# Kernel tuning notes

Measured on AMD Instinct MI355X. Metric: run time of the kernel, lower is better.

The kernel has to match this reference:

```python
import jax, jax.numpy as jnp
import numpy as np

B, P_LEN, Q_LEN, D, H = 16, 128, 256, 128, 128


def setup_inputs() -> dict:
    key = jax.random.key(0)
    ks = jax.random.split(key, 16)
    s = 0.05
    inp = {
        "p": jax.random.normal(ks[0], (B, P_LEN, D), dtype=jnp.float32),
        "q": jax.random.normal(ks[1], (B, Q_LEN, D), dtype=jnp.float32),
        # attention linears: W_s, W_t (D->H), W_r (H->H), W_e (H->1)
        "Ws_w": jax.random.normal(ks[2], (H, D), dtype=jnp.float32) * s,
        "Ws_b": jnp.zeros((H,), dtype=jnp.float32),
        "Wt_w": jax.random.normal(ks[3], (H, D), dtype=jnp.float32) * s,
        "Wt_b": jnp.zeros((H,), dtype=jnp.float32),
        "Wr_w": jax.random.normal(ks[4], (H, H), dtype=jnp.float32) * s,
        "Wr_b": jnp.zeros((H,), dtype=jnp.float32),
        "We_w": jax.random.normal(ks[5], (H,), dtype=jnp.float32) * s,
        "We_b": jax.random.normal(ks[6], (), dtype=jnp.float32) * s,
        # input gate linear: (D+H)->(D+H)
        "Wg_w": jax.random.normal(ks[7], (D + H, D + H), dtype=jnp.float32) * s,
        "Wg_b": jnp.zeros((D + H,), dtype=jnp.float32),
        # LSTMCell: gates ordered i,f,g,o as in torch
        "Wih": jax.random.normal(ks[8], (4 * H, D + H), dtype=jnp.float32) * s,
        "Whh": jax.random.normal(ks[9], (4 * H, H), dtype=jnp.float32) * s,
        "bih": jnp.zeros((4 * H,), dtype=jnp.float32),
        "bhh": jnp.zeros((4 * H,), dtype=jnp.float32),
        # entity_embedding=None -> these int ids are unused pass-throughs
        "p_seq": jax.random.randint(ks[10], (B, P_LEN), 0, 10000, dtype=jnp.int64) if jax.config.jax_enable_x64 else jax.random.randint(ks[10], (B, P_LEN), 0, 10000, dtype=jnp.int32),
        "q_seq": jax.random.randint(ks[11], (B, Q_LEN), 0, 10000, dtype=jnp.int32),
    }
    return inp


def _mlstm(p, q, Ws_w, Ws_b, Wt_w, Wt_b, Wr_w, Wr_b, We_w, We_b,
           Wg_w, Wg_b, Wih, Whh, bih, bhh):
    # precompute W_s(q): [B, Q, H] (loop-invariant)
    W_hs = jnp.einsum('bqd,hd->bqh', q, Ws_w) + Ws_b
    h0 = jnp.zeros((p.shape[0], H), dtype=p.dtype)
    c0 = jnp.zeros_like(h0)

    def step(carry, p_pos):  # p_pos: [B, D]
        h, c = carry
        # TriMatchAttention (entity_embedding=None)
        w_ht = p_pos @ Wt_w.T + Wt_b            # [B, H]
        w_hm = h @ Wr_w.T + Wr_b                # [B, H]
        s = jnp.tanh(W_hs + (w_ht + w_hm)[:, None, :])   # [B, Q, H]
        score = jnp.einsum('bqh,h->bq', s, We_w) + We_b  # [B, Q]
        a = jax.nn.softmax(score, axis=1)                # [B, Q]
        alpha = jnp.einsum('bq,bqh->bh', a, W_hs)        # [B, H]
        x = jnp.concatenate([alpha, p_pos], axis=1)      # [B, H+D]
        # gate (IsGate=True)
        g_t = jax.nn.sigmoid(x @ Wg_w.T + Wg_b)
        x = g_t * x
        # LSTMCell
        gates = x @ Wih.T + bih + h @ Whh.T + bhh        # [B, 4H]
        i, f, g, o = jnp.split(gates, 4, axis=1)
        c_new = jax.nn.sigmoid(f) * c + jax.nn.sigmoid(i) * jnp.tanh(g)
        h_new = jax.nn.sigmoid(o) * jnp.tanh(c_new)
        return (h_new, c_new), h_new

    _, hs = jax.lax.scan(step, (h0, c0), jnp.swapaxes(p, 0, 1))  # hs: [P, B, H]
    return jnp.swapaxes(hs, 0, 1)  # [B, P, H] == stacked h_states[1:]


def reference(p, q, Ws_w, Ws_b, Wt_w, Wt_b, Wr_w, Wr_b, We_w, We_b,
              Wg_w, Wg_b, Wih, Whh, bih, bhh, p_seq, q_seq):
    # p_seq/q_seq unused: entity_embedding=None in TriMatchAttention
    return _mlstm(p, q, Ws_w, Ws_b, Wt_w, Wt_b, Wr_w, Wr_b, We_w, We_b,
                  Wg_w, Wg_b, Wih, Whh, bih, bhh)
```

## Files before the change

### kernel.cpp

```cpp
#include <hip/hip_runtime.h>
#include <hip/hip_fp16.h>
#include <cstdint>


__device__ __forceinline__ float bf2f(uint16_t u) {
  uint32_t x = ((uint32_t)u) << 16; float f; __builtin_memcpy(&f, &x, 4); return f;
}
__device__ __forceinline__ float load_in(const void* p, size_t i, int f32) {
  return f32 ? ((const float*)p)[i] : bf2f(((const uint16_t*)p)[i]);
}
__device__ __forceinline__ float frcp(float x) { return __builtin_amdgcn_rcpf(x); }
__device__ __forceinline__ float tanh_fast(float x) {
  float E = __expf(2.0f * x);
  return 1.0f - 2.0f * frcp(E + 1.0f);
}
__device__ __forceinline__ float sigm(float x) { return frcp(1.0f + __expf(-x)); }
__device__ __forceinline__ float2 h2f(uint32_t u) {
  __half2 h; __builtin_memcpy(&h, &u, 4); return __half22float2(h);
}
__device__ __forceinline__ uint32_t f2h(float a, float b) {
  __half2 h = __floats2half2_rn(a, b);
  uint32_t u; __builtin_memcpy(&u, &h, 4); return u;
}

__global__ void detect_kernel(const uint16_t* __restrict__ q16,
                              uint32_t* __restrict__ flag) {
  __shared__ int cnt;
  if (threadIdx.x == 0) cnt = 0;
  __syncthreads();
  int bad = 0;
  for (int i = threadIdx.x; i < 4096; i += 256) {
    int e = (q16[i] >> 7) & 0xFF;
    if (e > 0x8A) bad++;
  }
  atomicAdd(&cnt, bad);
  __syncthreads();
  if (threadIdx.x == 0) *flag = (cnt > 16) ? 1u : 0u;
}

__global__ void pack2(const void* __restrict__ p,
                      const void* __restrict__ Wr,  const void* __restrict__ Wrb_,
                      const void* __restrict__ Wew_, const void* __restrict__ Web_,
                      const void* __restrict__ Wg,
                      const void* __restrict__ Wih, const void* __restrict__ Whh,
                      const void* __restrict__ bih, const void* __restrict__ bhh,
                      float* __restrict__ pf,
                      uint32_t* __restrict__ WrP, float* __restrict__ wrb,
                      float* __restrict__ wew, float* __restrict__ web,
                      uint32_t* __restrict__ WgP, uint32_t* __restrict__ WTP,
                      float* __restrict__ bbv,
                      const uint32_t* __restrict__ flag) {
  const int f32 = (int)*flag;
  long idx = (long)blockIdx.x * blockDim.x + threadIdx.x;
  if (idx < 262144) { pf[idx] = load_in(p, idx, f32); return; }
  idx -= 262144;
  if (idx < 8192) {
    int c = (int)(idx >> 2), w = (int)(idx & 3);
    int i = c >> 10, t = c & 1023;
    int jA = t >> 3, kgA = t & 7;
    int k = kgA * 16 + i * 8 + w * 2;
    WrP[idx] = f2h(load_in(Wr, (size_t)jA * 128 + k, f32),
                   load_in(Wr, (size_t)jA * 128 + k + 1, f32));
    return; }
  idx -= 8192;
  if (idx < 128) { wrb[idx] = load_in(Wrb_, idx, f32); return; }
  idx -= 128;
  if (idx < 128) { wew[idx] = load_in(Wew_, idx, f32); return; }
  idx -= 128;
  if (idx < 1) { web[0] = load_in(Web_, 0, f32); return; }
  idx -= 1;
  if (idx < 16384) {
    int c = (int)(idx >> 2), w = (int)(idx & 3);
    int i = c >> 10, t = c & 1023;
    int iE = t >> 2, kgE = t & 3;
    int k = kgE * 32 + i * 8 + w * 2;
    WgP[idx] = f2h(load_in(Wg, (size_t)iE * 256 + k, f32),
                   load_in(Wg, (size_t)iE * 256 + k + 1, f32));
    return; }
  idx -= 16384;
  if (idx < 98304) {
    int c = (int)(idx >> 2), w = (int)(idx & 3);
    int i = c >> 10, t = c & 1023;
    int iF = t >> 1, kgF = t & 1;
    int k = kgF * 192 + i * 8 + w * 2;
    float v0 = (k < 256) ? load_in(Wih, (size_t)iF * 256 + k, f32)
                         : load_in(Whh, (size_t)iF * 128 + (k - 256), f32);
    float v1 = (k + 1 < 256) ? load_in(Wih, (size_t)iF * 256 + k + 1, f32)
                             : load_in(Whh, (size_t)iF * 128 + (k + 1 - 256), f32);
    WTP[idx] = f2h(v0, v1);
    return; }
  idx -= 98304;
  if (idx < 512) { bbv[idx] = load_in(bih, idx, f32) + load_in(bhh, idx, f32); }
}

__global__ __launch_bounds__(256) void gemm3(
    const void* __restrict__ q, const void* __restrict__ p,
    const void* __restrict__ Wsw, const void* __restrict__ Wsb,
    const void* __restrict__ Wtw, const void* __restrict__ Wtb,
    const void* __restrict__ Wgw, const void* __restrict__ Wgb,
    float* __restrict__ whs, float* __restrict__ wht, float* __restrict__ Gp,
    const uint32_t* __restrict__ flag) {
  __shared__ float A_l[16][128];
  __shared__ float W_l[64][129];
  const int f32 = (int)*flag;
  const int t = threadIdx.x;
  const void* A; const void* W; const void* bias; float* out;
  int lda = 128, ldw, w_off, C, r0;
  int blk = blockIdx.x;
  if (blk < 256)      { A = q; W = Wsw; bias = Wsb; out = whs; ldw = 128; w_off = 0;   C = 128; r0 = blk * 16; }
  else if (blk < 384) { A = p; W = Wtw; bias = Wtb; out = wht; ldw = 128; w_off = 0;   C = 128; r0 = (blk - 256) * 16; }
  else                { A = p; W = Wgw; bias = Wgb; out = Gp;  ldw = 256; w_off = 128; C = 256; r0 = (blk - 384) * 16; }
  for (int idx = t; idx < 16 * 128; idx += 256) {
    int rr = idx >> 7, kk = idx & 127;
    A_l[rr][kk] = load_in(A, (size_t)(r0 + rr) * lda + kk, f32);
  }
  const int c_l = t & 63, rg = t >> 6;
  for (int c0 = 0; c0 < C; c0 += 64) {
    __syncthreads();
    for (int idx = t; idx < 64 * 128; idx += 256) {
      int cc = idx >> 7, kk = idx & 127;
      W_l[cc][kk] = load_in(W, (size_t)w_off + (size_t)(c0 + cc) * ldw + kk, f32);
    }
    __syncthreads();
    float acc[4] = {0.f, 0.f, 0.f, 0.f};
    for (int k = 0; k < 128; k++) {
      float w = W_l[c_l][k];
#pragma unroll
      for (int x = 0; x < 4; x++) acc[x] = fmaf(A_l[rg * 4 + x][k], w, acc[x]);
    }
    float bv = load_in(bias, c0 + c_l, f32);
#pragma unroll
    for (int x = 0; x < 4; x++)
      out[(size_t)(r0 + rg * 4 + x) * C + c0 + c_l] = acc[x] + bv;
  }
}

__global__ void tapack(const float* __restrict__ whs, uint32_t* __restrict__ TAp) {
  int o = blockIdx.x * 256 + threadIdx.x;
  int b = o >> 14, r = o & 16383;
  int c = r >> 2, w = r & 3;
  int i = c >> 10, t = c & 1023;
  int qB = t >> 2, hgB = t & 3;
  int h = hgB * 32 + i * 8 + w * 2;
  const float* base = whs + ((size_t)b * 256 + qB) * 128 + h;
  TAp[o] = f2h(tanhf(base[0]), tanhf(base[1]));
}

#define TUIDX(j) ((((j) >> 5) * 36) + ((j) & 31))
#define SCIDX(q) ((((q) >> 5) * 36) + ((q) & 31))
#define AIDX(h)  ((((h) >> 5) * 36) + ((h) & 31))
#define HIDX(k)  ((((k) >> 4) * 20) + ((k) & 15))

__global__ __launch_bounds__(1024) void mlstm_seq9(
    const float* __restrict__ pf,
    const float* __restrict__ whs,
    const float* __restrict__ wht_g,
    const float* __restrict__ Gp_g,
    const uint32_t* __restrict__ WrP,
    const float* __restrict__ wrb,
    const float* __restrict__ wew,
    const float* __restrict__ web,
    const uint32_t* __restrict__ WgP,
    const uint32_t* __restrict__ WTP,
    const uint32_t* __restrict__ TAp,
    const float* __restrict__ bbv,
    float* __restrict__ out) {
  const int b = blockIdx.x, t = threadIdx.x;

  __shared__ __align__(16) float whs_l[256 * 132];
  __shared__ __align__(16) float tu_s[144];
  __shared__ __align__(16) float wew_s[144];
  __shared__ __align__(16) float sc_s[288];
  __shared__ __align__(16) float e_s[256];
  __shared__ __align__(16) float alpha_s[144];
  __shared__ __align__(16) float xh_s[384];
  __shared__ __align__(16) float h_s[160];
  __shared__ __align__(16) float gates_s[512];
  __shared__ float inv_s;

  const float* whs_b = whs + (size_t)b * 32768;

  const int jA = t >> 3, kgA = t & 7;
  const int qB = t >> 2, hgB = t & 3;
  const int hD = t >> 3, qgD = t & 7;
  const int iE = t >> 2, kgE = t & 3;
  const int iF = t >> 1, kgF = t & 1;

  for (int i4 = t; i4 < 8192; i4 += 1024)
    *(float4*)(whs_l + (i4 >> 5) * 132 + ((i4 & 31) << 2)) =
        *(const float4*)(whs_b + ((size_t)i4 << 2));
  if (t < 128) wew_s[TUIDX(t)] = wew[t];
  if (t < 160) h_s[t] = 0.f;
  if (t < 128) xh_s[256 + t] = 0.f;

  const float wrb_r = wrb[jA];
  const float web_r = web[0];
  const float bbF_r = bbv[iF];
  float c_r = 0.f;

  const uint4* wrp4 = (const uint4*)WrP;
  const uint4* wgp4 = (const uint4*)WgP;
  const uint4* wtp4 = (const uint4*)WTP;
  const uint4* tap4 = (const uint4*)TAp + (size_t)b * 4096;

  float wht_c = (kgA == 0) ? wht_g[((size_t)b * 128 + 0) * 128 + jA] : 0.f;
  float gp_c  = (kgE == 0) ? Gp_g[((size_t)b * 128 + 0) * 256 + iE] : 0.f;
  float pf_c  = (kgE == 0 && iE >= 128) ? pf[((size_t)b * 128 + 0) * 128 + (iE - 128)] : 0.f;

  __syncthreads();

  for (int st = 0; st < 128; st++) {
    const int st1 = (st < 127) ? st + 1 : 127;
    float wht_n = (kgA == 0) ? wht_g[((size_t)b * 128 + st1) * 128 + jA] : 0.f;
    float gp_n  = (kgE == 0) ? Gp_g[((size_t)b * 128 + st1) * 256 + iE] : 0.f;
    float pf_n  = (kgE == 0 && iE >= 128) ? pf[((size_t)b * 128 + st1) * 128 + (iE - 128)] : 0.f;

    {
      float acc = 0.f;
#pragma unroll
      for (int i = 0; i < 2; i++) {
        uint4 wv = wrp4[i * 1024 + t];
        const float* hp = h_s + kgA * 20 + i * 8;
        float4 hA = *(const float4*)(hp);
        float4 hB = *(const float4*)(hp + 4);
        float2 w0 = h2f(wv.x), w1 = h2f(wv.y), w2 = h2f(wv.z), w3 = h2f(wv.w);
        acc = fmaf(hA.x, w0.x, acc); acc = fmaf(hA.y, w0.y, acc);
        acc = fmaf(hA.z, w1.x, acc); acc = fmaf(hA.w, w1.y, acc);
        acc = fmaf(hB.x, w2.x, acc); acc = fmaf(hB.y, w2.y, acc);
        acc = fmaf(hB.z, w3.x, acc); acc = fmaf(hB.w, w3.y, acc);
      }
      acc += __shfl_xor(acc, 1);
      acc += __shfl_xor(acc, 2);
      acc += __shfl_xor(acc, 4);
      if (kgA == 0) tu_s[TUIDX(jA)] = tanh_fast(acc + wrb_r + wht_c);
    }
    __syncthreads();

    {
      float acc = 0.f;
#pragma unroll
      for (int i = 0; i < 4; i++) {
        uint4 av = tap4[i * 1024 + t];
        const float* up = tu_s + hgB * 36 + i * 8;
        const float* wp = wew_s + hgB * 36 + i * 8;
        float4 uA = *(const float4*)(up);
        float4 uB = *(const float4*)(up + 4);
        float4 wA = *(const float4*)(wp);
        float4 wB = *(const float4*)(wp + 4);
        float2 a0 = h2f(av.x), a1 = h2f(av.y), a2 = h2f(av.z), a3 = h2f(av.w);
        acc = fmaf((a0.x + uA.x) * frcp(fmaxf(fmaf(a0.x, uA.x, 1.f), 1e-6f)), wA.x, acc);
        acc = fmaf((a0.y + uA.y) * frcp(fmaxf(fmaf(a0.y, uA.y, 1.f), 1e-6f)), wA.y, acc);
        acc = fmaf((a1.x + uA.z) * frcp(fmaxf(fmaf(a1.x, uA.z, 1.f), 1e-6f)), wA.z, acc);
        acc = fmaf((a1.y + uA.w) * frcp(fmaxf(fmaf(a1.y, uA.w, 1.f), 1e-6f)), wA.w, acc);
        acc = fmaf((a2.x + uB.x) * frcp(fmaxf(fmaf(a2.x, uB.x, 1.f), 1e-6f)), wB.x, acc);
        acc = fmaf((a2.y + uB.y) * frcp(fmaxf(fmaf(a2.y, uB.y, 1.f), 1e-6f)), wB.y, acc);
        acc = fmaf((a3.x + uB.z) * frcp(fmaxf(fmaf(a3.x, uB.z, 1.f), 1e-6f)), wB.z, acc);
        acc = fmaf((a3.y + uB.w) * frcp(fmaxf(fmaf(a3.y, uB.w, 1.f), 1e-6f)), wB.w, acc);
      }
      acc += __shfl_xor(acc, 1);
      acc += __shfl_xor(acc, 2);
      if (hgB == 0) sc_s[SCIDX(qB)] = acc + web_r;
    }
    __syncthreads();

    if (t < 64) {
      float s0 = sc_s[SCIDX(t)],       s1 = sc_s[SCIDX(t + 64)];
      float s2 = sc_s[SCIDX(t + 128)], s3 = sc_s[SCIDX(t + 192)];
      float mx = fmaxf(fmaxf(s0, s1), fmaxf(s2, s3));
#pragma unroll
      for (int d = 1; d < 64; d <<= 1) mx = fmaxf(mx, __shfl_xor(mx, d));
      float e0 = __expf(s0 - mx), e1 = __expf(s1 - mx),
            e2 = __expf(s2 - mx), e3 = __expf(s3 - mx);
      float sum = e0 + e1 + e2 + e3;
#pragma unroll
      for (int d = 1; d < 64; d <<= 1) sum += __shfl_xor(sum, d);
      e_s[t] = e0; e_s[t + 64] = e1; e_s[t + 128] = e2; e_s[t + 192] = e3;
      if (t == 0) inv_s = frcp(sum);
    }
    __syncthreads();

    {
      const float* whs_p = whs_l + qgD * 132 + hD;
      float acc = 0.f;
#pragma unroll 8
      for (int r = 0; r < 32; r++)
        acc = fmaf(e_s[qgD + 8 * r], whs_p[r * 1056], acc);
      acc += __shfl_xor(acc, 1);
      acc += __shfl_xor(acc, 2);
      acc += __shfl_xor(acc, 4);
      if (qgD == 0) alpha_s[AIDX(hD)] = acc * inv_s;
    }
    __syncthreads();

    {
      float acc = 0.f;
#pragma unroll
      for (int i = 0; i < 4; i++) {
        uint4 wv = wgp4[i * 1024 + t];
        const float* ap = alpha_s + kgE * 36 + i * 8;
        float4 aA = *(const float4*)(ap);
        float4 aB = *(const float4*)(ap + 4);
        float2 w0 = h2f(wv.x), w1 = h2f(wv.y), w2 = h2f(wv.z), w3 = h2f(wv.w);
        acc = fmaf(aA.x, w0.x, acc); acc = fmaf(aA.y, w0.y, acc);
        acc = fmaf(aA.z, w1.x, acc); acc = fmaf(aA.w, w1.y, acc);
        acc = fmaf(aB.x, w2.x, acc); acc = fmaf(aB.y, w2.y, acc);
        acc = fmaf(aB.z, w3.x, acc); acc = fmaf(aB.w, w3.y, acc);
      }
      acc += __shfl_xor(acc, 1);
      acc += __shfl_xor(acc, 2);
      if (kgE == 0) {
        float sg = sigm(gp_c + acc);
        float xv = (iE < 128) ? alpha_s[AIDX(iE)] : pf_c;
        xh_s[iE] = sg * xv;
      }
    }
    __syncthreads();

    {
      const float* xb = xh_s + kgF * 192;
      float acc = 0.f;
#pragma unroll 8
      for (int i = 0; i < 24; i++) {
        uint4 wv = wtp4[i * 1024 + t];
        float4 xA = *(const float4*)(xb + i * 8);
        float4 xB = *(const float4*)(xb + i * 8 + 4);
        float2 w0 = h2f(wv.x), w1 = h2f(wv.y), w2 = h2f(wv.z), w3 = h2f(wv.w);
        acc = fmaf(xA.x, w0.x, acc); acc = fmaf(xA.y, w0.y, acc);
        acc = fmaf(xA.z, w1.x, acc); acc = fmaf(xA.w, w1.y, acc);
        acc = fmaf(xB.x, w2.x, acc); acc = fmaf(xB.y, w2.y, acc);
        acc = fmaf(xB.z, w3.x, acc); acc = fmaf(xB.w, w3.y, acc);
      }
      acc += __shfl_xor(acc, 1);
      if (kgF == 0) gates_s[iF] = acc + bbF_r;
    }
    __syncthreads();

    if (t < 128) {
      float iv = sigm(gates_s[t]);
      float fv = sigm(gates_s[128 + t]);
      float gv = tanh_fast(gates_s[256 + t]);
      float ov = sigm(gates_s[384 + t]);
      float cn = fmaf(fv, c_r, iv * gv);
      float hn = ov * tanh_fast(cn);
      c_r = cn;
      h_s[HIDX(t)] = hn;
      xh_s[256 + t] = hn;
      out[((size_t)b * 128 + st) * 128 + t] = hn;
    }
    __syncthreads();

    wht_c = wht_n; gp_c = gp_n; pf_c = pf_n;
  }
}

extern "C" void kernel_launch(void* const* d_in, const int* in_sizes, int n_in,
                              void* d_out, int out_size, void* d_ws, size_t ws_size,
                              hipStream_t stream) {
  static const int SZ_DICT[18] = {262144, 524288, 16384, 128, 16384, 128,
                                  16384, 128, 128, 1, 65536, 256,
                                  131072, 65536, 512, 512, 2048, 4096};
  static const int ALPHA2DICT[18] = {9, 8, 11, 10, 13, 12, 7, 6, 3, 2, 5, 4,
                                     15, 14, 0, 16, 1, 17};
  const void* in[18];
  for (int i = 0; i < 18; i++) in[i] = (i < n_in) ? d_in[i] : nullptr;

  bool dict_ok = true;
  int lim = (n_in < 16) ? n_in : 16;
  for (int i = 0; i < lim; i++) if (in_sizes[i] != SZ_DICT[i]) dict_ok = false;
  if (!dict_ok) {
    bool alpha_ok = true;
    for (int s = 0; s < n_in && s < 18; s++)
      if (in_sizes[s] != SZ_DICT[ALPHA2DICT[s]]) alpha_ok = false;
    if (alpha_ok)
      for (int s = 0; s < n_in && s < 18; s++) in[ALPHA2DICT[s]] = d_in[s];
  }

  const void* p   = in[0];  const void* q   = in[1];
  const void* Wsw = in[2];  const void* Wsb = in[3];
  const void* Wtw = in[4];  const void* Wtb = in[5];
  const void* Wrw = in[6];  const void* Wrb = in[7];
  const void* Wew = in[8];  const void* Web = in[9];
  const void* Wgw = in[10]; const void* Wgb = in[11];
  const void* Wih = in[12]; const void* Whh = in[13];
  const void* bih = in[14]; const void* bhh = in[15];

  float* ws = (float*)d_ws;
  float* whs  = ws;
  float* pff  = whs + 524288;
  float* wht  = pff + 262144;
  float* Gp   = wht + 262144;
  uint32_t* WrP = (uint32_t*)(Gp + 524288);
  uint32_t* WgP = WrP + 8192;
  uint32_t* WTP = WgP + 16384;
  uint32_t* TAp = WTP + 98304;
  float* bbv  = (float*)(TAp + 262144);
  float* wrb  = bbv + 512;
  float* wew  = wrb + 128;
  float* web  = wew + 128;
  uint32_t* flag = (uint32_t*)(web + 4);

  hipLaunchKernelGGL(detect_kernel, dim3(1), dim3(256), 0, stream,
                     (const uint16_t*)q, flag);
  hipLaunchKernelGGL(pack2, dim3(1508), dim3(256), 0, stream,
                     p, Wrw, Wrb, Wew, Web, Wgw, Wih, Whh, bih, bhh,
                     pff, WrP, wrb, wew, web, WgP, WTP, bbv, flag);
  hipLaunchKernelGGL(gemm3, dim3(512), dim3(256), 0, stream,
                     q, p, Wsw, Wsb, Wtw, Wtb, Wgw, Wgb, whs, wht, Gp, flag);
  hipLaunchKernelGGL(tapack, dim3(1024), dim3(256), 0, stream, whs, TAp);
  hipLaunchKernelGGL(mlstm_seq9, dim3(16), dim3(1024), 0, stream,
                     pff, whs, wht, Gp, WrP, wrb, wew, web, WgP, WTP, TAp, bbv,
                     (float*)d_out);
}
```

Baseline: 1.420 ms.

## Pack W_hs to fp16 in global, cache LSTM weights in LDS, use fdot2

The sequential kernel no longer stages fp32 W_hs in LDS. It reads a pre-packed fp16 copy (DWp, produced by the extended pack kernel) for the alpha reduction. The freed LDS holds 9 of the 24 LSTM weight chunks, and the remaining chunks are software-prefetched from global. The gate input vector is stored as half2 so the LSTM matvec can use packed fp16 dot2 instructions. This cuts per-step global and LDS traffic and ALU work on the serial critical path, at the cost of fp16 rounding of activations and an extra packing pass.

```diff
diff --git a/kernel.cpp b/kernel.cpp
--- a/kernel.cpp
+++ b/kernel.cpp
@@ -21,6 +21,22 @@
 __device__ __forceinline__ uint32_t f2h(float a, float b) {
   __half2 h = __floats2half2_rn(a, b);
   uint32_t u; __builtin_memcpy(&u, &h, 4); return u;
+}
+
+typedef _Float16 h2v __attribute__((ext_vector_type(2)));
+__device__ __forceinline__ float dot2(uint32_t w, uint32_t x, float acc) {
+#if defined(__has_builtin)
+#if __has_builtin(__builtin_amdgcn_fdot2)
+  h2v a, b; __builtin_memcpy(&a, &w, 4); __builtin_memcpy(&b, &x, 4);
+  return __builtin_amdgcn_fdot2(a, b, acc, false);
+#else
+  float2 af = h2f(w), bf = h2f(x);
+  return fmaf(af.x, bf.x, fmaf(af.y, bf.y, acc));
+#endif
+#else
+  float2 af = h2f(w), bf = h2f(x);
+  return fmaf(af.x, bf.x, fmaf(af.y, bf.y, acc));
+#endif
 }
 
 __global__ void detect_kernel(const uint16_t* __restrict__ q16,
@@ -135,15 +151,27 @@
   }
 }
 
-__global__ void tapack(const float* __restrict__ whs, uint32_t* __restrict__ TAp) {
+__global__ void actpack(const float* __restrict__ whs,
+                        uint32_t* __restrict__ TAp, uint32_t* __restrict__ DWp) {
   int o = blockIdx.x * 256 + threadIdx.x;
-  int b = o >> 14, r = o & 16383;
-  int c = r >> 2, w = r & 3;
-  int i = c >> 10, t = c & 1023;
-  int qB = t >> 2, hgB = t & 3;
-  int h = hgB * 32 + i * 8 + w * 2;
-  const float* base = whs + ((size_t)b * 256 + qB) * 128 + h;
-  TAp[o] = f2h(tanhf(base[0]), tanhf(base[1]));
+  if (o < 262144) {
+    int b = o >> 14, r = o & 16383;
+    int c = r >> 2, w = r & 3;
+    int i = c >> 10, t = c & 1023;
+    int qB = t >> 2, hgB = t & 3;
+    int h = hgB * 32 + i * 8 + w * 2;
+    const float* base = whs + ((size_t)b * 256 + qB) * 128 + h;
+    TAp[o] = f2h(tanhf(base[0]), tanhf(base[1]));
+  } else {
+    o -= 262144;
+    int b = o >> 14, r2 = o & 16383;
+    int i = r2 >> 12, r = r2 & 4095;
+    int t = r >> 2, w = r & 3;
+    int qgD = t & 7, hD = t >> 3;
+    int q0 = qgD + 64 * i + 16 * w;
+    const float* base = whs + (size_t)b * 32768;
+    DWp[o] = f2h(base[(size_t)q0 * 128 + hD], base[(size_t)(q0 + 8) * 128 + hD]);
+  }
 }
 
 #define TUIDX(j) ((((j) >> 5) * 36) + ((j) & 31))
@@ -151,9 +179,8 @@
 #define AIDX(h)  ((((h) >> 5) * 36) + ((h) & 31))
 #define HIDX(k)  ((((k) >> 4) * 20) + ((k) & 15))
 
-__global__ __launch_bounds__(1024) void mlstm_seq9(
+__global__ __launch_bounds__(1024) void mlstm_seq10(
     const float* __restrict__ pf,
-    const float* __restrict__ whs,
     const float* __restrict__ wht_g,
     const float* __restrict__ Gp_g,
     const uint32_t* __restrict__ WrP,
@@ -163,22 +190,21 @@
     const uint32_t* __restrict__ WgP,
     const uint32_t* __restrict__ WTP,
     const uint32_t* __restrict__ TAp,
+    const uint32_t* __restrict__ DWp,
     const float* __restrict__ bbv,
     float* __restrict__ out) {
   const int b = blockIdx.x, t = threadIdx.x;
 
-  __shared__ __align__(16) float whs_l[256 * 132];
+  __shared__ __align__(16) uint4 lds_wt4[9 * 1024];
+  __shared__ __align__(16) uint32_t xh_h2[192];
   __shared__ __align__(16) float tu_s[144];
   __shared__ __align__(16) float wew_s[144];
   __shared__ __align__(16) float sc_s[288];
   __shared__ __align__(16) float e_s[256];
   __shared__ __align__(16) float alpha_s[144];
-  __shared__ __align__(16) float xh_s[384];
   __shared__ __align__(16) float h_s[160];
   __shared__ __align__(16) float gates_s[512];
   __shared__ float inv_s;
-
-  const float* whs_b = whs + (size_t)b * 32768;
 
   const int jA = t >> 3, kgA = t & 7;
   const int qB = t >> 2, hgB = t & 3;
@@ -186,22 +212,21 @@
   const int iE = t >> 2, kgE = t & 3;
   const int iF = t >> 1, kgF = t & 1;
 
-  for (int i4 = t; i4 < 8192; i4 += 1024)
-    *(float4*)(whs_l + (i4 >> 5) * 132 + ((i4 & 31) << 2)) =
-        *(const float4*)(whs_b + ((size_t)i4 << 2));
+  const uint4* wrp4 = (const uint4*)WrP;
+  const uint4* wgp4 = (const uint4*)WgP;
+  const uint4* wtp4 = (const uint4*)WTP;
+  const uint4* tap4 = (const uint4*)TAp + (size_t)b * 4096;
+  const uint4* dwp4 = (const uint4*)DWp + (size_t)b * 4096;
+
+  for (int i = t; i < 9216; i += 1024) lds_wt4[i] = wtp4[i];
   if (t < 128) wew_s[TUIDX(t)] = wew[t];
   if (t < 160) h_s[t] = 0.f;
-  if (t < 128) xh_s[256 + t] = 0.f;
+  if (t < 64) xh_h2[128 + t] = 0u;
 
   const float wrb_r = wrb[jA];
   const float web_r = web[0];
   const float bbF_r = bbv[iF];
   float c_r = 0.f;
-
-  const uint4* wrp4 = (const uint4*)WrP;
-  const uint4* wgp4 = (const uint4*)WgP;
-  const uint4* wtp4 = (const uint4*)WTP;
-  const uint4* tap4 = (const uint4*)TAp + (size_t)b * 4096;
 
   float wht_c = (kgA == 0) ? wht_g[((size_t)b * 128 + 0) * 128 + jA] : 0.f;
   float gp_c  = (kgE == 0) ? Gp_g[((size_t)b * 128 + 0) * 256 + iE] : 0.f;
@@ -280,11 +305,17 @@
     __syncthreads();
 
     {
-      const float* whs_p = whs_l + qgD * 132 + hD;
       float acc = 0.f;
-#pragma unroll 8
-      for (int r = 0; r < 32; r++)
-        acc = fmaf(e_s[qgD + 8 * r], whs_p[r * 1056], acc);
+#pragma unroll
+      for (int i = 0; i < 4; i++) {
+        uint4 v = dwp4[i * 1024 + t];
+        float2 s0 = h2f(v.x), s1 = h2f(v.y), s2 = h2f(v.z), s3 = h2f(v.w);
+        const float* ep = e_s + qgD + 64 * i;
+        acc = fmaf(ep[0],  s0.x, acc); acc = fmaf(ep[8],  s0.y, acc);
+        acc = fmaf(ep[16], s1.x, acc); acc = fmaf(ep[24], s1.y, acc);
+        acc = fmaf(ep[32], s2.x, acc); acc = fmaf(ep[40], s2.y, acc);
+        acc = fmaf(ep[48], s3.x, acc); acc = fmaf(ep[56], s3.y, acc);
+      }
       acc += __shfl_xor(acc, 1);
       acc += __shfl_xor(acc, 2);
       acc += __shfl_xor(acc, 4);
@@ -308,27 +339,37 @@
       }
       acc += __shfl_xor(acc, 1);
       acc += __shfl_xor(acc, 2);
+      float v = 0.f;
       if (kgE == 0) {
         float sg = sigm(gp_c + acc);
         float xv = (iE < 128) ? alpha_s[AIDX(iE)] : pf_c;
-        xh_s[iE] = sg * xv;
-      }
+        v = sg * xv;
+      }
+      float vp = __shfl_xor(v, 4);
+      if (kgE == 0 && (iE & 1) == 0) xh_h2[iE >> 1] = f2h(v, vp);
     }
     __syncthreads();
 
     {
-      const float* xb = xh_s + kgF * 192;
+      const uint4* xv4 = (const uint4*)xh_h2;
       float acc = 0.f;
-#pragma unroll 8
-      for (int i = 0; i < 24; i++) {
-        uint4 wv = wtp4[i * 1024 + t];
-        float4 xA = *(const float4*)(xb + i * 8);
-        float4 xB = *(const float4*)(xb + i * 8 + 4);
-        float2 w0 = h2f(wv.x), w1 = h2f(wv.y), w2 = h2f(wv.z), w3 = h2f(wv.w);
-        acc = fmaf(xA.x, w0.x, acc); acc = fmaf(xA.y, w0.y, acc);
-        acc = fmaf(xA.z, w1.x, acc); acc = fmaf(xA.w, w1.y, acc);
-        acc = fmaf(xB.x, w2.x, acc); acc = fmaf(xB.y, w2.y, acc);
-        acc = fmaf(xB.z, w3.x, acc); acc = fmaf(xB.w, w3.y, acc);
+      uint4 pfb[4];
+#pragma unroll
+      for (int j = 0; j < 4; j++) pfb[j] = wtp4[(9 + j) * 1024 + t];
+#pragma unroll
+      for (int i = 0; i < 9; i++) {
+        uint4 wv = lds_wt4[i * 1024 + t];
+        uint4 xv = xv4[kgF * 24 + i];
+        acc = dot2(wv.x, xv.x, acc); acc = dot2(wv.y, xv.y, acc);
+        acc = dot2(wv.z, xv.z, acc); acc = dot2(wv.w, xv.w, acc);
+      }
+#pragma unroll
+      for (int i = 9; i < 24; i++) {
+        uint4 wv = pfb[(i - 9) & 3];
+        if (i + 4 < 24) pfb[(i - 9) & 3] = wtp4[(i + 4) * 1024 + t];
+        uint4 xv = xv4[kgF * 24 + i];
+        acc = dot2(wv.x, xv.x, acc); acc = dot2(wv.y, xv.y, acc);
+        acc = dot2(wv.z, xv.z, acc); acc = dot2(wv.w, xv.w, acc);
       }
       acc += __shfl_xor(acc, 1);
       if (kgF == 0) gates_s[iF] = acc + bbF_r;
@@ -344,7 +385,8 @@
       float hn = ov * tanh_fast(cn);
       c_r = cn;
       h_s[HIDX(t)] = hn;
-      xh_s[256 + t] = hn;
+      float hp = __shfl_xor(hn, 1);
+      if ((t & 1) == 0) xh_h2[128 + (t >> 1)] = f2h(hn, hp);
       out[((size_t)b * 128 + st) * 128 + t] = hn;
     }
     __syncthreads();
@@ -393,7 +435,8 @@
   uint32_t* WgP = WrP + 8192;
   uint32_t* WTP = WgP + 16384;
   uint32_t* TAp = WTP + 98304;
-  float* bbv  = (float*)(TAp + 262144);
+  uint32_t* DWp = TAp + 262144;
+  float* bbv  = (float*)(DWp + 262144);
   float* wrb  = bbv + 512;
   float* wew  = wrb + 128;
   float* web  = wew + 128;
@@ -406,8 +449,8 @@
                      pff, WrP, wrb, wew, web, WgP, WTP, bbv, flag);
   hipLaunchKernelGGL(gemm3, dim3(512), dim3(256), 0, stream,
                      q, p, Wsw, Wsb, Wtw, Wtb, Wgw, Wgb, whs, wht, Gp, flag);
-  hipLaunchKernelGGL(tapack, dim3(1024), dim3(256), 0, stream, whs, TAp);
-  hipLaunchKernelGGL(mlstm_seq9, dim3(16), dim3(1024), 0, stream,
-                     pff, whs, wht, Gp, WrP, wrb, wew, web, WgP, WTP, TAp, bbv,
+  hipLaunchKernelGGL(actpack, dim3(2048), dim3(256), 0, stream, whs, TAp, DWp);
+  hipLaunchKernelGGL(mlstm_seq10, dim3(16), dim3(1024), 0, stream,
+                     pff, wht, Gp, WrP, wrb, wew, web, WgP, WTP, TAp, DWp, bbv,
                      (float*)d_out);
 }
```

Measured after the change: 1.967 ms. 1.39x slower.
